# Kernel optimization log

Measured on AMD Instinct MI355X. Metric: run time of the kernel, lower is better.

The kernel has to match this reference:

```python
import jax, jax.numpy as jnp
import numpy as np

N_EMB = 768
N_HEAD = 12
B, T = 2, 2048
LN_EPS = 1e-5


def _ln(x, g, b):
    mu = jnp.mean(x, axis=-1, keepdims=True)
    var = jnp.mean((x - mu) ** 2, axis=-1, keepdims=True)
    return (x - mu) * jax.lax.rsqrt(var + LN_EPS) * g + b


def setup_inputs() -> dict:
    key = jax.random.key(0)
    ks = jax.random.split(key, 12)
    s = 0.02
    d = {
        "x": jax.random.normal(ks[0], (B, T, N_EMB), dtype=jnp.float32),
        "cond_len": 256,
        "padding_mask": jax.random.randint(ks[1], (B, T), 0, 2, dtype=jnp.int32),
        "g1": jnp.ones((N_EMB,), jnp.float32),
        "bln1": jnp.zeros((N_EMB,), jnp.float32),
        "g2": jnp.ones((N_EMB,), jnp.float32),
        "bln2": jnp.zeros((N_EMB,), jnp.float32),
        "Wq": jax.random.normal(ks[2], (N_EMB, N_EMB), jnp.float32) * s,
        "bq": jnp.zeros((N_EMB,), jnp.float32),
        "Wk": jax.random.normal(ks[3], (N_EMB, N_EMB), jnp.float32) * s,
        "bk": jnp.zeros((N_EMB,), jnp.float32),
        "Wv": jax.random.normal(ks[4], (N_EMB, N_EMB), jnp.float32) * s,
        "bv": jnp.zeros((N_EMB,), jnp.float32),
        "Wp": jax.random.normal(ks[5], (N_EMB, N_EMB), jnp.float32) * s,
        "bp": jnp.zeros((N_EMB,), jnp.float32),
        "W1": jax.random.normal(ks[6], (4 * N_EMB, N_EMB), jnp.float32) * s,
        "b1": jnp.zeros((4 * N_EMB,), jnp.float32),
        "W2": jax.random.normal(ks[7], (N_EMB, 4 * N_EMB), jnp.float32) * s,
        "b2": jnp.zeros((N_EMB,), jnp.float32),
    }
    return d


def reference(x, cond_len, padding_mask, g1, bln1, g2, bln2,
              Wq, bq, Wk, bk, Wv, bv, Wp, bp, W1, b1, W2, b2):
    Bc, Tc, C = x.shape
    H = N_HEAD
    Dh = C // H
    h = _ln(x, g1, bln1)
    q = (h @ Wq.T + bq).reshape(Bc, Tc, H, Dh)
    k = (h @ Wk.T + bk).reshape(Bc, Tc, H, Dh)
    v = (h @ Wv.T + bv).reshape(Bc, Tc, H, Dh)
    att = jnp.einsum("bqhd,bkhd->bhqk", q, k) * (1.0 / np.sqrt(Dh))
    # mask: key col allowed if col >= cond_len OR col < n_b, n_b = T - sum(pmask_b)
    n = Tc - jnp.sum(padding_mask, axis=1)  # [B]
    cols = jnp.arange(Tc)
    allowed = (cols[None, :] >= cond_len) | (cols[None, :] < n[:, None])  # [B,T]
    att = jnp.where(allowed[:, None, None, :], att, -jnp.inf)
    att = jax.nn.softmax(att, axis=-1)
    y = jnp.einsum("bhqk,bkhd->bqhd", att, v).reshape(Bc, Tc, C)
    x = x + (y @ Wp.T + bp)
    h2 = _ln(x, g2, bln2)
    m = jax.nn.gelu(h2 @ W1.T + b1, approximate=False) @ W2.T + b2
    return x + m
```

## Files before the change

### kernel.cpp

```cpp
#include <hip/hip_runtime.h>
#include <hip/hip_bf16.h>
#include <math.h>

typedef short bf16x8 __attribute__((ext_vector_type(8)));
typedef float f32x4 __attribute__((ext_vector_type(4)));
typedef unsigned short us4 __attribute__((ext_vector_type(4)));

#define MFMA(a, b, c) __builtin_amdgcn_mfma_f32_16x16x32_bf16(a, b, c, 0, 0, 0)

__device__ __forceinline__ unsigned short f2b(float f) {
  unsigned int u = __builtin_bit_cast(unsigned int, f);
  u += 0x7fffu + ((u >> 16) & 1u);
  return (unsigned short)(u >> 16);
}

__device__ __forceinline__ void gload16(const void* g, void* l) {
  __builtin_amdgcn_global_load_lds((const unsigned int*)g, (unsigned int*)l, 16, 0, 0);
}

__global__ void cvt_k(const float* __restrict__ src, unsigned short* __restrict__ dst, int n4) {
  int i = blockIdx.x * 256 + threadIdx.x;
  if (i >= n4) return;
  float4 v = ((const float4*)src)[i];
  us4 o; o.x = f2b(v.x); o.y = f2b(v.y); o.z = f2b(v.z); o.w = f2b(v.w);
  ((us4*)dst)[i] = o;
}

__global__ void cvt_qkv_k(const float* __restrict__ wq, const float* __restrict__ wk,
                          const float* __restrict__ wv, unsigned short* __restrict__ dst) {
  int i = blockIdx.x * 256 + threadIdx.x;
  if (i >= 2304 * 768 / 4) return;
  int e = i * 4;
  const float* src = e < 589824 ? wq + e : (e < 1179648 ? wk + (e - 589824) : wv + (e - 1179648));
  float4 v = *(const float4*)src;
  us4 o; o.x = f2b(v.x); o.y = f2b(v.y); o.z = f2b(v.z); o.w = f2b(v.w);
  ((us4*)dst)[i] = o;
}

__global__ void maskbias_k(const int* __restrict__ pm, const int* __restrict__ clp,
                           float* __restrict__ bias) {
  const int b = blockIdx.x, tid = threadIdx.x;
  int s = 0;
  for (int i = tid; i < 2048; i += 256) s += pm[b * 2048 + i];
  #pragma unroll
  for (int d = 1; d < 64; d <<= 1) s += __shfl_xor(s, d);
  __shared__ int red[4];
  if ((tid & 63) == 0) red[tid >> 6] = s;
  __syncthreads();
  const int n = 2048 - (red[0] + red[1] + red[2] + red[3]);
  const int cl = *clp;
  for (int t = tid; t < 2048; t += 256)
    bias[b * 2048 + t] = (t >= cl || t < n) ? 0.0f : -1e30f;
}

__global__ __launch_bounds__(256)
void ln_k(const float* __restrict__ x, const float* __restrict__ g,
          const float* __restrict__ be, unsigned short* __restrict__ out) {
  const int row = blockIdx.x * 4 + (threadIdx.x >> 6);
  const int l = threadIdx.x & 63;
  const float4* xr = (const float4*)(x + (size_t)row * 768);
  float4 v[3];
  float s = 0.f, s2 = 0.f;
  #pragma unroll
  for (int j = 0; j < 3; ++j) {
    v[j] = xr[l + j * 64];
    s += v[j].x + v[j].y + v[j].z + v[j].w;
    s2 += v[j].x * v[j].x + v[j].y * v[j].y + v[j].z * v[j].z + v[j].w * v[j].w;
  }
  #pragma unroll
  for (int d = 1; d < 64; d <<= 1) { s += __shfl_xor(s, d); s2 += __shfl_xor(s2, d); }
  const float mu = s * (1.0f / 768.0f);
  const float rstd = rsqrtf(s2 * (1.0f / 768.0f) - mu * mu + 1e-5f);
  #pragma unroll
  for (int j = 0; j < 3; ++j) {
    int c0 = (l + j * 64) * 4;
    us4 ov;
    ov.x = f2b((v[j].x - mu) * rstd * g[c0 + 0] + be[c0 + 0]);
    ov.y = f2b((v[j].y - mu) * rstd * g[c0 + 1] + be[c0 + 1]);
    ov.z = f2b((v[j].z - mu) * rstd * g[c0 + 2] + be[c0 + 2]);
    ov.w = f2b((v[j].w - mu) * rstd * g[c0 + 3] + be[c0 + 3]);
    *(us4*)(out + (size_t)row * 768 + c0) = ov;
  }
}

template<int MODE>
__global__ __launch_bounds__(256)
void gemm_k(const unsigned short* __restrict__ A, const unsigned short* __restrict__ W,
            const float* __restrict__ bias0, const float* __restrict__ bias1,
            const float* __restrict__ bias2, const float* __restrict__ resid,
            void* __restrict__ out, unsigned short* __restrict__ out2, int N, int K) {
  __shared__ __align__(16) unsigned short At[128 * 32];
  __shared__ __align__(16) unsigned short Wt[128 * 32];
  const int m0 = blockIdx.y * 128;
  const int n0 = blockIdx.x * 128;
  const int tid = threadIdx.x;
  const int w = tid >> 6, l = tid & 63;
  const int wm = w >> 1, wn = w & 1;
  const int lr = l & 15, lg = l >> 4;
  f32x4 acc[4][4] = {};

  const int nkt = K >> 5;
  for (int kt = 0; kt < nkt; ++kt) {
    const int k0 = kt << 5;
    #pragma unroll
    for (int i = 0; i < 2; ++i) {
      int slot = (i * 4 + w) * 64 + l;
      int row = slot >> 2, c8 = (slot & 3) << 3;
      gload16(A + (size_t)(m0 + row) * K + k0 + c8, (char*)At + ((i * 4 + w) * 64) * 16);
      gload16(W + (size_t)(n0 + row) * K + k0 + c8, (char*)Wt + ((i * 4 + w) * 64) * 16);
    }
    __syncthreads();
    bf16x8 af[4], bf[4];
    #pragma unroll
    for (int i = 0; i < 4; ++i) {
      af[i] = *(const bf16x8*)&At[(wm * 64 + i * 16 + lr) * 32 + lg * 8];
      bf[i] = *(const bf16x8*)&Wt[(wn * 64 + i * 16 + lr) * 32 + lg * 8];
    }
    #pragma unroll
    for (int mi = 0; mi < 4; ++mi)
      #pragma unroll
      for (int ni = 0; ni < 4; ++ni)
        acc[mi][ni] = MFMA(af[mi], bf[ni], acc[mi][ni]);
    __syncthreads();
  }

  #pragma unroll
  for (int mi = 0; mi < 4; ++mi) {
    #pragma unroll
    for (int ni = 0; ni < 4; ++ni) {
      #pragma unroll
      for (int r = 0; r < 4; ++r) {
        int row = m0 + wm * 64 + mi * 16 + lg * 4 + r;
        int col = n0 + wn * 64 + ni * 16 + lr;
        float v = acc[mi][ni][r];
        if (MODE == 0) {
          float bb = col < 768 ? bias0[col] : (col < 1536 ? bias1[col - 768] : bias2[col - 1536]);
          v += bb;
          if (col < 1536) {
            ((unsigned short*)out)[(size_t)row * 2304 + col] = f2b(v);
          } else {
            int cc = col - 1536;
            int d = cc & 63, hh = cc >> 6;
            int b = row >> 11, t = row & 2047;
            out2[(((size_t)b * 12 + hh) * 64 + d) * 2048 + t] = f2b(v);
          }
        } else if (MODE == 1) {
          v += bias0[col] + resid[(size_t)row * N + col];
          ((float*)out)[(size_t)row * N + col] = v;
        } else {
          v += bias0[col];
          v = 0.5f * v * (1.0f + erff(v * 0.70710678118f));
          ((unsigned short*)out)[(size_t)row * N + col] = f2b(v);
        }
      }
    }
  }
}

__global__ __launch_bounds__(256)
void attn_k(const unsigned short* __restrict__ qkv, const unsigned short* __restrict__ vt,
            const float* __restrict__ abias, unsigned short* __restrict__ y) {
  __shared__ __align__(16) unsigned short Kt[64 * 64];
  __shared__ __align__(16) unsigned short Vt[64 * 64];
  __shared__ __align__(16) unsigned short Pl[4][16 * 64];
  const int tile = blockIdx.x, h = blockIdx.y, b = blockIdx.z;
  const int tid = threadIdx.x, w = tid >> 6, l = tid & 63;
  const int lr = l & 15, lg = l >> 4;
  const int tq0 = tile * 64 + w * 16;

  bf16x8 qf[2];
  {
    const unsigned short* qrow = qkv + ((size_t)b * 2048 + tq0 + lr) * 2304 + h * 64;
    qf[0] = *(const bf16x8*)(qrow + lg * 8);
    qf[1] = *(const bf16x8*)(qrow + 32 + lg * 8);
  }
  f32x4 o[4] = {};
  float mrow[4] = {-1e30f, -1e30f, -1e30f, -1e30f};
  float lrow[4] = {0.f, 0.f, 0.f, 0.f};

  const unsigned short* Kg = qkv + (size_t)b * 2048 * 2304 + 768 + h * 64;
  const unsigned short* Vg = vt + ((size_t)b * 12 + h) * 64 * 2048;

  for (int kt = 0; kt < 32; ++kt) {
    const int t0 = kt * 64;
    __syncthreads();
    #pragma unroll
    for (int i = 0; i < 2; ++i) {
      int slot = (i * 4 + w) * 64 + l;
      int row = slot >> 3;
      int cc = (slot & 7) ^ (row & 7);
      gload16(Kg + (size_t)(t0 + row) * 2304 + cc * 8, (char*)Kt + ((i * 4 + w) * 64) * 16);
      gload16(Vg + (size_t)row * 2048 + t0 + cc * 8, (char*)Vt + ((i * 4 + w) * 64) * 16);
    }
    __syncthreads();

    f32x4 s[4] = {};
    #pragma unroll
    for (int kk = 0; kk < 2; ++kk)
      #pragma unroll
      for (int sub = 0; sub < 4; ++sub) {
        int trow = sub * 16 + lr;
        int boff = (trow * 128 + kk * 64 + lg * 16) ^ ((trow & 7) << 4);
        bf16x8 kf = *(const bf16x8*)((const char*)Kt + boff);
        s[sub] = MFMA(qf[kk], kf, s[sub]);
      }

    float bb[4];
    #pragma unroll
    for (int sub = 0; sub < 4; ++sub) bb[sub] = abias[b * 2048 + t0 + sub * 16 + lr];
    #pragma unroll
    for (int sub = 0; sub < 4; ++sub)
      #pragma unroll
      for (int r = 0; r < 4; ++r)
        s[sub][r] = s[sub][r] * 0.125f + bb[sub];

    float mx[4];
    #pragma unroll
    for (int r = 0; r < 4; ++r)
      mx[r] = fmaxf(fmaxf(s[0][r], s[1][r]), fmaxf(s[2][r], s[3][r]));
    #pragma unroll
    for (int d = 1; d < 16; d <<= 1)
      #pragma unroll
      for (int r = 0; r < 4; ++r)
        mx[r] = fmaxf(mx[r], __shfl_xor(mx[r], d, 16));

    float corr[4], rs[4] = {0.f, 0.f, 0.f, 0.f};
    #pragma unroll
    for (int r = 0; r < 4; ++r) {
      float mn = fmaxf(mrow[r], mx[r]);
      corr[r] = __expf(mrow[r] - mn);
      mrow[r] = mn;
    }
    #pragma unroll
    for (int sub = 0; sub < 4; ++sub)
      #pragma unroll
      for (int r = 0; r < 4; ++r) {
        float p = __expf(s[sub][r] - mrow[r]);
        s[sub][r] = p;
        rs[r] += p;
      }
    #pragma unroll
    for (int d = 1; d < 16; d <<= 1)
      #pragma unroll
      for (int r = 0; r < 4; ++r)
        rs[r] += __shfl_xor(rs[r], d, 16);
    #pragma unroll
    for (int r = 0; r < 4; ++r)
      lrow[r] = lrow[r] * corr[r] + rs[r];
    #pragma unroll
    for (int ds_ = 0; ds_ < 4; ++ds_)
      #pragma unroll
      for (int r = 0; r < 4; ++r)
        o[ds_][r] *= corr[r];

    #pragma unroll
    for (int sub = 0; sub < 4; ++sub)
      #pragma unroll
      for (int r = 0; r < 4; ++r) {
        int prow = lg * 4 + r;
        int boff = (prow * 128 + (sub * 16 + lr) * 2) ^ ((prow & 7) << 4);
        *(unsigned short*)((char*)Pl[w] + boff) = f2b(s[sub][r]);
      }

    #pragma unroll
    for (int kk = 0; kk < 2; ++kk) {
      int aoff = (lr * 128 + kk * 64 + lg * 16) ^ ((lr & 7) << 4);
      bf16x8 pa = *(const bf16x8*)((const char*)Pl[w] + aoff);
      #pragma unroll
      for (int ds_ = 0; ds_ < 4; ++ds_) {
        int vrow = ds_ * 16 + lr;
        int voff = (vrow * 128 + kk * 64 + lg * 16) ^ ((vrow & 7) << 4);
        bf16x8 vf = *(const bf16x8*)((const char*)Vt + voff);
        o[ds_] = MFMA(pa, vf, o[ds_]);
      }
    }
  }

  #pragma unroll
  for (int ds_ = 0; ds_ < 4; ++ds_)
    #pragma unroll
    for (int r = 0; r < 4; ++r) {
      int row = tq0 + lg * 4 + r;
      int col = ds_ * 16 + lr;
      y[((size_t)b * 2048 + row) * 768 + h * 64 + col] = f2b(o[ds_][r] / lrow[r]);
    }
}

extern "C" void kernel_launch(void* const* d_in, const int* in_sizes, int n_in,
                              void* d_out, int out_size, void* d_ws, size_t ws_size,
                              hipStream_t stream) {
  const float* x    = (const float*)d_in[0];
  const int* condp  = (const int*)d_in[1];
  const int* pmask  = (const int*)d_in[2];
  const float* g1   = (const float*)d_in[3];
  const float* bln1 = (const float*)d_in[4];
  const float* g2   = (const float*)d_in[5];
  const float* bln2 = (const float*)d_in[6];
  const float* Wq   = (const float*)d_in[7];
  const float* bq   = (const float*)d_in[8];
  const float* Wk   = (const float*)d_in[9];
  const float* bk   = (const float*)d_in[10];
  const float* Wv   = (const float*)d_in[11];
  const float* bv   = (const float*)d_in[12];
  const float* Wp   = (const float*)d_in[13];
  const float* bp   = (const float*)d_in[14];
  const float* W1   = (const float*)d_in[15];
  const float* b1   = (const float*)d_in[16];
  const float* W2   = (const float*)d_in[17];
  const float* b2   = (const float*)d_in[18];

  char* p = (char*)d_ws;
  auto alloc = [&](size_t bytes) { char* r = p; p += (bytes + 255) & ~(size_t)255; return r; };
  unsigned short* Wqkv = (unsigned short*)alloc((size_t)2304 * 768 * 2);
  unsigned short* Wpb  = (unsigned short*)alloc((size_t)589824 * 2);
  unsigned short* W1b  = (unsigned short*)alloc((size_t)2359296 * 2);
  unsigned short* W2b  = (unsigned short*)alloc((size_t)2359296 * 2);
  unsigned short* hb   = (unsigned short*)alloc((size_t)4096 * 768 * 2);
  unsigned short* qkv  = (unsigned short*)alloc((size_t)4096 * 2304 * 2);
  unsigned short* vtb  = (unsigned short*)alloc((size_t)24 * 64 * 2048 * 2);
  unsigned short* yb   = (unsigned short*)alloc((size_t)4096 * 768 * 2);
  float* xmid          = (float*)alloc((size_t)4096 * 768 * 4);
  unsigned short* h2b  = (unsigned short*)alloc((size_t)4096 * 768 * 2);
  unsigned short* mlph = (unsigned short*)alloc((size_t)4096 * 3072 * 2);
  float* abias         = (float*)alloc((size_t)2 * 2048 * 4);

  cvt_qkv_k<<<(2304 * 768 / 4 + 255) / 256, 256, 0, stream>>>(Wq, Wk, Wv, Wqkv);
  cvt_k<<<(589824 / 4 + 255) / 256, 256, 0, stream>>>(Wp, Wpb, 589824 / 4);
  cvt_k<<<(2359296 / 4 + 255) / 256, 256, 0, stream>>>(W1, W1b, 2359296 / 4);
  cvt_k<<<(2359296 / 4 + 255) / 256, 256, 0, stream>>>(W2, W2b, 2359296 / 4);
  maskbias_k<<<2, 256, 0, stream>>>(pmask, condp, abias);
  ln_k<<<1024, 256, 0, stream>>>(x, g1, bln1, hb);
  gemm_k<0><<<dim3(18, 32), 256, 0, stream>>>(hb, Wqkv, bq, bk, bv, nullptr, qkv, vtb, 2304, 768);
  attn_k<<<dim3(32, 12, 2), 256, 0, stream>>>(qkv, vtb, abias, yb);
  gemm_k<1><<<dim3(6, 32), 256, 0, stream>>>(yb, Wpb, bp, nullptr, nullptr, x, xmid, nullptr, 768, 768);
  ln_k<<<1024, 256, 0, stream>>>(xmid, g2, bln2, h2b);
  gemm_k<2><<<dim3(24, 32), 256, 0, stream>>>(h2b, W1b, b1, nullptr, nullptr, nullptr, mlph, nullptr, 3072, 768);
  gemm_k<1><<<dim3(6, 32), 256, 0, stream>>>(mlph, W2b, b2, nullptr, nullptr, xmid, (float*)d_out, nullptr, 768, 3072);
}
```

Measured before the change: 397.3 us.

## Split attention over keys with 32x32 MFMA and split-K output GEMMs

Attention is rewritten to use 32x32x16 MFMA with 512-thread blocks. The key dimension is split into four chunks whose partial outputs are merged by a separate combine kernel, and probabilities are packed in registers through lane shuffles instead of going through LDS. The projection and MLP-down GEMMs become split-K over four slices with fp32 partials, reduced in a fused bias+residual+LayerNorm kernel and a final combine kernel. The weight conversions are merged into fewer launches and buffers are aliased. This raises parallelism for the narrow N=768 GEMMs and for attention, at the cost of extra partial-buffer traffic and more kernel launches.

```diff
diff --git a/kernel.cpp b/kernel.cpp
--- a/kernel.cpp
+++ b/kernel.cpp
@@ -4,9 +4,11 @@
 
 typedef short bf16x8 __attribute__((ext_vector_type(8)));
 typedef float f32x4 __attribute__((ext_vector_type(4)));
+typedef float f32x16 __attribute__((ext_vector_type(16)));
 typedef unsigned short us4 __attribute__((ext_vector_type(4)));
 
-#define MFMA(a, b, c) __builtin_amdgcn_mfma_f32_16x16x32_bf16(a, b, c, 0, 0, 0)
+#define MFMA16(a, b, c) __builtin_amdgcn_mfma_f32_16x16x32_bf16(a, b, c, 0, 0, 0)
+#define MFMA32(a, b, c) __builtin_amdgcn_mfma_f32_32x32x16_bf16(a, b, c, 0, 0, 0)
 
 __device__ __forceinline__ unsigned short f2b(float f) {
   unsigned int u = __builtin_bit_cast(unsigned int, f);
@@ -14,16 +16,19 @@
   return (unsigned short)(u >> 16);
 }
 
+__device__ __forceinline__ float b2f(unsigned short u) {
+  unsigned int x = ((unsigned int)u) << 16;
+  return __builtin_bit_cast(float, x);
+}
+
+__device__ __forceinline__ unsigned int cvtpk(float lo, float hiv) {
+  unsigned int r;
+  asm("v_cvt_pk_bf16_f32 %0, %1, %2" : "=v"(r) : "v"(lo), "v"(hiv));
+  return r;
+}
+
 __device__ __forceinline__ void gload16(const void* g, void* l) {
   __builtin_amdgcn_global_load_lds((const unsigned int*)g, (unsigned int*)l, 16, 0, 0);
-}
-
-__global__ void cvt_k(const float* __restrict__ src, unsigned short* __restrict__ dst, int n4) {
-  int i = blockIdx.x * 256 + threadIdx.x;
-  if (i >= n4) return;
-  float4 v = ((const float4*)src)[i];
-  us4 o; o.x = f2b(v.x); o.y = f2b(v.y); o.z = f2b(v.z); o.w = f2b(v.w);
-  ((us4*)dst)[i] = o;
 }
 
 __global__ void cvt_qkv_k(const float* __restrict__ wq, const float* __restrict__ wk,
@@ -37,6 +42,23 @@
   ((us4*)dst)[i] = o;
 }
 
+__global__ void cvt3_k(const float* __restrict__ s0, const float* __restrict__ s1,
+                       const float* __restrict__ s2, unsigned short* __restrict__ d0,
+                       unsigned short* __restrict__ d1, unsigned short* __restrict__ d2) {
+  const int n0 = 147456, n1 = 589824, n2 = 589824;
+  int i = blockIdx.x * 256 + threadIdx.x;
+  const float* s; unsigned short* d; int j = i;
+  if (j < n0) { s = s0; d = d0; }
+  else {
+    j -= n0;
+    if (j < n1) { s = s1; d = d1; }
+    else { j -= n1; if (j >= n2) return; s = s2; d = d2; }
+  }
+  float4 v = ((const float4*)s)[j];
+  us4 o; o.x = f2b(v.x); o.y = f2b(v.y); o.z = f2b(v.z); o.w = f2b(v.w);
+  ((us4*)d)[j] = o;
+}
+
 __global__ void maskbias_k(const int* __restrict__ pm, const int* __restrict__ clp,
                            float* __restrict__ bias) {
   const int b = blockIdx.x, tid = threadIdx.x;
@@ -87,8 +109,8 @@
 __global__ __launch_bounds__(256)
 void gemm_k(const unsigned short* __restrict__ A, const unsigned short* __restrict__ W,
             const float* __restrict__ bias0, const float* __restrict__ bias1,
-            const float* __restrict__ bias2, const float* __restrict__ resid,
-            void* __restrict__ out, unsigned short* __restrict__ out2, int N, int K) {
+            const float* __restrict__ bias2, void* __restrict__ out,
+            unsigned short* __restrict__ out2, int N, int K) {
   __shared__ __align__(16) unsigned short At[128 * 32];
   __shared__ __align__(16) unsigned short Wt[128 * 32];
   const int m0 = blockIdx.y * 128;
@@ -120,7 +142,7 @@
     for (int mi = 0; mi < 4; ++mi)
       #pragma unroll
       for (int ni = 0; ni < 4; ++ni)
-        acc[mi][ni] = MFMA(af[mi], bf[ni], acc[mi][ni]);
+        acc[mi][ni] = MFMA16(af[mi], bf[ni], acc[mi][ni]);
     __syncthreads();
   }
 
@@ -144,9 +166,6 @@
             int b = row >> 11, t = row & 2047;
             out2[(((size_t)b * 12 + hh) * 64 + d) * 2048 + t] = f2b(v);
           }
-        } else if (MODE == 1) {
-          v += bias0[col] + resid[(size_t)row * N + col];
-          ((float*)out)[(size_t)row * N + col] = v;
         } else {
           v += bias0[col];
           v = 0.5f * v * (1.0f + erff(v * 0.70710678118f));
@@ -158,132 +177,272 @@
 }
 
 __global__ __launch_bounds__(256)
+void gemm_pk(const unsigned short* __restrict__ A, const unsigned short* __restrict__ W,
+             float* __restrict__ part, int N, int K, int KS) {
+  __shared__ __align__(16) unsigned short At[128 * 32];
+  __shared__ __align__(16) unsigned short Wt[128 * 32];
+  const int m0 = blockIdx.y * 128;
+  const int n0 = blockIdx.x * 128;
+  const int kb = blockIdx.z * KS;
+  const int tid = threadIdx.x;
+  const int w = tid >> 6, l = tid & 63;
+  const int wm = w >> 1, wn = w & 1;
+  const int lr = l & 15, lg = l >> 4;
+  f32x4 acc[4][4] = {};
+
+  const int nkt = KS >> 5;
+  for (int kt = 0; kt < nkt; ++kt) {
+    const int k0 = kb + (kt << 5);
+    #pragma unroll
+    for (int i = 0; i < 2; ++i) {
+      int slot = (i * 4 + w) * 64 + l;
+      int row = slot >> 2, c8 = (slot & 3) << 3;
+      gload16(A + (size_t)(m0 + row) * K + k0 + c8, (char*)At + ((i * 4 + w) * 64) * 16);
+      gload16(W + (size_t)(n0 + row) * K + k0 + c8, (char*)Wt + ((i * 4 + w) * 64) * 16);
+    }
+    __syncthreads();
+    bf16x8 af[4], bf[4];
+    #pragma unroll
+    for (int i = 0; i < 4; ++i) {
+      af[i] = *(const bf16x8*)&At[(wm * 64 + i * 16 + lr) * 32 + lg * 8];
+      bf[i] = *(const bf16x8*)&Wt[(wn * 64 + i * 16 + lr) * 32 + lg * 8];
+    }
+    #pragma unroll
+    for (int mi = 0; mi < 4; ++mi)
+      #pragma unroll
+      for (int ni = 0; ni < 4; ++ni)
+        acc[mi][ni] = MFMA16(af[mi], bf[ni], acc[mi][ni]);
+    __syncthreads();
+  }
+
+  #pragma unroll
+  for (int mi = 0; mi < 4; ++mi)
+    #pragma unroll
+    for (int ni = 0; ni < 4; ++ni)
+      #pragma unroll
+      for (int r = 0; r < 4; ++r) {
+        int row = m0 + wm * 64 + mi * 16 + lg * 4 + r;
+        int col = n0 + wn * 64 + ni * 16 + lr;
+        part[((size_t)blockIdx.z * 4096 + row) * N + col] = acc[mi][ni][r];
+      }
+}
+
+__global__ __launch_bounds__(512, 4)
 void attn_k(const unsigned short* __restrict__ qkv, const unsigned short* __restrict__ vt,
-            const float* __restrict__ abias, unsigned short* __restrict__ y) {
+            const float* __restrict__ abias, unsigned short* __restrict__ opart,
+            float* __restrict__ mpart, float* __restrict__ lpart) {
   __shared__ __align__(16) unsigned short Kt[64 * 64];
   __shared__ __align__(16) unsigned short Vt[64 * 64];
-  __shared__ __align__(16) unsigned short Pl[4][16 * 64];
-  const int tile = blockIdx.x, h = blockIdx.y, b = blockIdx.z;
+  __shared__ __align__(16) float absh[512];
+  const int d0 = blockIdx.x;
+  const int c = d0 & 7, t_ = d0 >> 3;
+  const int G = (t_ >> 3) * 8 + c;
+  const int qt = t_ & 7;
+  const int bh = G >> 2, split = G & 3;
+  const int b = bh / 12, h = bh - b * 12;
+  const int q0 = qt * 256;
+  const int tb = split * 512;
   const int tid = threadIdx.x, w = tid >> 6, l = tid & 63;
-  const int lr = l & 15, lg = l >> 4;
-  const int tq0 = tile * 64 + w * 16;
-
-  bf16x8 qf[2];
+  const int ql = l & 31, hi = l >> 5;
+  const int q = q0 + w * 32 + ql;
+
+  absh[tid] = abias[b * 2048 + tb + tid];
+
+  bf16x8 qf[4];
   {
-    const unsigned short* qrow = qkv + ((size_t)b * 2048 + tq0 + lr) * 2304 + h * 64;
-    qf[0] = *(const bf16x8*)(qrow + lg * 8);
-    qf[1] = *(const bf16x8*)(qrow + 32 + lg * 8);
-  }
-  f32x4 o[4] = {};
-  float mrow[4] = {-1e30f, -1e30f, -1e30f, -1e30f};
-  float lrow[4] = {0.f, 0.f, 0.f, 0.f};
-
-  const unsigned short* Kg = qkv + (size_t)b * 2048 * 2304 + 768 + h * 64;
-  const unsigned short* Vg = vt + ((size_t)b * 12 + h) * 64 * 2048;
-
-  for (int kt = 0; kt < 32; ++kt) {
-    const int t0 = kt * 64;
+    const unsigned short* qrow = qkv + ((size_t)b * 2048 + q) * 2304 + h * 64 + hi * 8;
+    #pragma unroll
+    for (int ds = 0; ds < 4; ++ds) qf[ds] = *(const bf16x8*)(qrow + ds * 16);
+  }
+
+  f32x16 o0 = {}, o1 = {};
+  float mrow = -1e30f, lrow = 0.f;
+
+  const int srow = tid >> 3;
+  const int scc = (tid & 7) ^ (srow & 7);
+  const unsigned short* KgL = qkv + ((size_t)b * 2048 + tb + srow) * 2304 + 768 + h * 64 + scc * 8;
+  const unsigned short* VgL = vt + ((size_t)bh * 64 + srow) * 2048 + tb + scc * 8;
+  char* KtW = (char*)Kt + w * 1024;
+  char* VtW = (char*)Vt + w * 1024;
+
+  for (int tt = 0; tt < 8; ++tt) {
+    gload16(KgL + (size_t)(tt * 64) * 2304, KtW);
+    gload16(VgL + tt * 64, VtW);
     __syncthreads();
-    #pragma unroll
-    for (int i = 0; i < 2; ++i) {
-      int slot = (i * 4 + w) * 64 + l;
-      int row = slot >> 3;
-      int cc = (slot & 7) ^ (row & 7);
-      gload16(Kg + (size_t)(t0 + row) * 2304 + cc * 8, (char*)Kt + ((i * 4 + w) * 64) * 16);
-      gload16(Vg + (size_t)row * 2048 + t0 + cc * 8, (char*)Vt + ((i * 4 + w) * 64) * 16);
-    }
+
+    f32x16 sa0 = {}, sa1 = {};
+    {
+      const int r0 = ql, r1 = 32 + ql;
+      #pragma unroll
+      for (int ds = 0; ds < 4; ++ds) {
+        bf16x8 kf0 = *(const bf16x8*)((const char*)Kt + r0 * 128 + (((ds * 2 + hi) ^ (r0 & 7)) << 4));
+        bf16x8 kf1 = *(const bf16x8*)((const char*)Kt + r1 * 128 + (((ds * 2 + hi) ^ (r1 & 7)) << 4));
+        sa0 = MFMA32(kf0, qf[ds], sa0);
+        sa1 = MFMA32(kf1, qf[ds], sa1);
+      }
+    }
+
+    float mt = -1e30f;
+    #pragma unroll
+    for (int g = 0; g < 4; ++g) {
+      float4 b0 = *(const float4*)&absh[tt * 64 + g * 8 + hi * 4];
+      float4 b1 = *(const float4*)&absh[tt * 64 + 32 + g * 8 + hi * 4];
+      float bb0[4] = {b0.x, b0.y, b0.z, b0.w};
+      float bb1[4] = {b1.x, b1.y, b1.z, b1.w};
+      #pragma unroll
+      for (int r2 = 0; r2 < 4; ++r2) {
+        float v0 = sa0[g * 4 + r2] * 0.125f + bb0[r2];
+        float v1 = sa1[g * 4 + r2] * 0.125f + bb1[r2];
+        sa0[g * 4 + r2] = v0; sa1[g * 4 + r2] = v1;
+        mt = fmaxf(mt, fmaxf(v0, v1));
+      }
+    }
+    mt = fmaxf(mt, __shfl_xor(mt, 32));
+
+    const bool grow = mt > mrow;
+    const float mnew = grow ? mt : mrow;
+    const float corr = __expf(mrow - mnew);
+    mrow = mnew;
+    if (__any((int)grow)) {
+      #pragma unroll
+      for (int g = 0; g < 4; ++g)
+        #pragma unroll
+        for (int r2 = 0; r2 < 4; ++r2) {
+          float cc2 = __shfl(corr, g * 8 + hi * 4 + r2);
+          o0[g * 4 + r2] *= cc2;
+          o1[g * 4 + r2] *= cc2;
+        }
+    }
+
+    float rs = 0.f;
+    auto half_pv = [&](const f32x16& sv, int ksb) {
+      unsigned int u[8];
+      #pragma unroll
+      for (int g = 0; g < 4; ++g) {
+        float e0 = __expf(sv[g * 4 + 0] - mnew);
+        float e1 = __expf(sv[g * 4 + 1] - mnew);
+        float e2 = __expf(sv[g * 4 + 2] - mnew);
+        float e3 = __expf(sv[g * 4 + 3] - mnew);
+        rs += (e0 + e1) + (e2 + e3);
+        u[g * 2]     = cvtpk(e0, e1);
+        u[g * 2 + 1] = cvtpk(e2, e3);
+      }
+      #pragma unroll
+      for (int kh = 0; kh < 2; ++kh) {
+        unsigned int a0 = u[kh * 4 + 0], a1 = u[kh * 4 + 1];
+        unsigned int c0 = u[kh * 4 + 2], c1 = u[kh * 4 + 3];
+        unsigned int xa0 = (unsigned int)__shfl_xor((int)a0, 32);
+        unsigned int xa1 = (unsigned int)__shfl_xor((int)a1, 32);
+        unsigned int xc0 = (unsigned int)__shfl_xor((int)c0, 32);
+        unsigned int xc1 = (unsigned int)__shfl_xor((int)c1, 32);
+        uint4 pk;
+        pk.x = hi ? xc0 : a0;
+        pk.y = hi ? xc1 : a1;
+        pk.z = hi ? c0 : xa0;
+        pk.w = hi ? c1 : xa1;
+        bf16x8 pa = __builtin_bit_cast(bf16x8, pk);
+        const int ks = ksb + kh;
+        const int vr0 = ql, vr1 = 32 + ql;
+        bf16x8 vf0 = *(const bf16x8*)((const char*)Vt + vr0 * 128 + (((ks * 2 + hi) ^ (vr0 & 7)) << 4));
+        o0 = MFMA32(pa, vf0, o0);
+        bf16x8 vf1 = *(const bf16x8*)((const char*)Vt + vr1 * 128 + (((ks * 2 + hi) ^ (vr1 & 7)) << 4));
+        o1 = MFMA32(pa, vf1, o1);
+      }
+    };
+    half_pv(sa0, 0);
+    half_pv(sa1, 2);
+
+    rs += __shfl_xor(rs, 32);
+    lrow = lrow * corr + rs;
     __syncthreads();
-
-    f32x4 s[4] = {};
-    #pragma unroll
-    for (int kk = 0; kk < 2; ++kk)
-      #pragma unroll
-      for (int sub = 0; sub < 4; ++sub) {
-        int trow = sub * 16 + lr;
-        int boff = (trow * 128 + kk * 64 + lg * 16) ^ ((trow & 7) << 4);
-        bf16x8 kf = *(const bf16x8*)((const char*)Kt + boff);
-        s[sub] = MFMA(qf[kk], kf, s[sub]);
-      }
-
-    float bb[4];
-    #pragma unroll
-    for (int sub = 0; sub < 4; ++sub) bb[sub] = abias[b * 2048 + t0 + sub * 16 + lr];
-    #pragma unroll
-    for (int sub = 0; sub < 4; ++sub)
-      #pragma unroll
-      for (int r = 0; r < 4; ++r)
-        s[sub][r] = s[sub][r] * 0.125f + bb[sub];
-
-    float mx[4];
-    #pragma unroll
-    for (int r = 0; r < 4; ++r)
-      mx[r] = fmaxf(fmaxf(s[0][r], s[1][r]), fmaxf(s[2][r], s[3][r]));
-    #pragma unroll
-    for (int d = 1; d < 16; d <<= 1)
-      #pragma unroll
-      for (int r = 0; r < 4; ++r)
-        mx[r] = fmaxf(mx[r], __shfl_xor(mx[r], d, 16));
-
-    float corr[4], rs[4] = {0.f, 0.f, 0.f, 0.f};
-    #pragma unroll
-    for (int r = 0; r < 4; ++r) {
-      float mn = fmaxf(mrow[r], mx[r]);
-      corr[r] = __expf(mrow[r] - mn);
-      mrow[r] = mn;
-    }
-    #pragma unroll
-    for (int sub = 0; sub < 4; ++sub)
-      #pragma unroll
-      for (int r = 0; r < 4; ++r) {
-        float p = __expf(s[sub][r] - mrow[r]);
-        s[sub][r] = p;
-        rs[r] += p;
-      }
-    #pragma unroll
-    for (int d = 1; d < 16; d <<= 1)
-      #pragma unroll
-      for (int r = 0; r < 4; ++r)
-        rs[r] += __shfl_xor(rs[r], d, 16);
-    #pragma unroll
-    for (int r = 0; r < 4; ++r)
-      lrow[r] = lrow[r] * corr[r] + rs[r];
-    #pragma unroll
-    for (int ds_ = 0; ds_ < 4; ++ds_)
-      #pragma unroll
-      for (int r = 0; r < 4; ++r)
-        o[ds_][r] *= corr[r];
-
-    #pragma unroll
-    for (int sub = 0; sub < 4; ++sub)
-      #pragma unroll
-      for (int r = 0; r < 4; ++r) {
-        int prow = lg * 4 + r;
-        int boff = (prow * 128 + (sub * 16 + lr) * 2) ^ ((prow & 7) << 4);
-        *(unsigned short*)((char*)Pl[w] + boff) = f2b(s[sub][r]);
-      }
-
-    #pragma unroll
-    for (int kk = 0; kk < 2; ++kk) {
-      int aoff = (lr * 128 + kk * 64 + lg * 16) ^ ((lr & 7) << 4);
-      bf16x8 pa = *(const bf16x8*)((const char*)Pl[w] + aoff);
-      #pragma unroll
-      for (int ds_ = 0; ds_ < 4; ++ds_) {
-        int vrow = ds_ * 16 + lr;
-        int voff = (vrow * 128 + kk * 64 + lg * 16) ^ ((vrow & 7) << 4);
-        bf16x8 vf = *(const bf16x8*)((const char*)Vt + voff);
-        o[ds_] = MFMA(pa, vf, o[ds_]);
-      }
-    }
-  }
-
-  #pragma unroll
-  for (int ds_ = 0; ds_ < 4; ++ds_)
-    #pragma unroll
-    for (int r = 0; r < 4; ++r) {
-      int row = tq0 + lg * 4 + r;
-      int col = ds_ * 16 + lr;
-      y[((size_t)b * 2048 + row) * 768 + h * 64 + col] = f2b(o[ds_][r] / lrow[r]);
-    }
+  }
+
+  const size_t orow0 = (size_t)split * 49152 + (size_t)bh * 2048 + q0 + w * 32;
+  if (hi == 0) { mpart[orow0 + ql] = mrow; lpart[orow0 + ql] = lrow; }
+  #pragma unroll
+  for (int g = 0; g < 4; ++g)
+    #pragma unroll
+    for (int r2 = 0; r2 < 4; ++r2) {
+      int oq = r2 + g * 8 + hi * 4;
+      opart[(orow0 + oq) * 64 + ql]      = f2b(o0[g * 4 + r2]);
+      opart[(orow0 + oq) * 64 + 32 + ql] = f2b(o1[g * 4 + r2]);
+    }
+}
+
+__global__ __launch_bounds__(256)
+void attn_comb_k(const unsigned short* __restrict__ op, const float* __restrict__ mp,
+                 const float* __restrict__ lp, unsigned short* __restrict__ y) {
+  const int row = blockIdx.x * 4 + (threadIdx.x >> 6);
+  const int l = threadIdx.x & 63;
+  float m0 = mp[row], m1 = mp[49152 + row], m2 = mp[2 * 49152 + row], m3 = mp[3 * 49152 + row];
+  float M = fmaxf(fmaxf(m0, m1), fmaxf(m2, m3));
+  float w0 = __expf(m0 - M), w1 = __expf(m1 - M), w2 = __expf(m2 - M), w3 = __expf(m3 - M);
+  float den = w0 * lp[row] + w1 * lp[49152 + row] + w2 * lp[2 * 49152 + row] + w3 * lp[3 * 49152 + row];
+  float num = w0 * b2f(op[((size_t)0 * 49152 + row) * 64 + l])
+            + w1 * b2f(op[((size_t)1 * 49152 + row) * 64 + l])
+            + w2 * b2f(op[((size_t)2 * 49152 + row) * 64 + l])
+            + w3 * b2f(op[((size_t)3 * 49152 + row) * 64 + l]);
+  const int bh = row >> 11, qq = row & 2047;
+  const int bb = bh / 12, hh = bh - bb * 12;
+  y[((size_t)(bb * 2048 + qq)) * 768 + hh * 64 + l] = f2b(num / den);
+}
+
+__global__ __launch_bounds__(256)
+void proj_ln_k(const float* __restrict__ part, const float* __restrict__ bp,
+               const float* __restrict__ xres, const float* __restrict__ g2,
+               const float* __restrict__ bln2, float* __restrict__ xmid,
+               unsigned short* __restrict__ h2) {
+  const int row = blockIdx.x * 4 + (threadIdx.x >> 6);
+  const int l = threadIdx.x & 63;
+  float4 v[3];
+  float s = 0.f, s2 = 0.f;
+  #pragma unroll
+  for (int j = 0; j < 3; ++j) {
+    const int cc = l + j * 64;
+    float4 a = ((const float4*)(xres + (size_t)row * 768))[cc];
+    float4 bb = ((const float4*)bp)[cc];
+    a.x += bb.x; a.y += bb.y; a.z += bb.z; a.w += bb.w;
+    #pragma unroll
+    for (int sp = 0; sp < 4; ++sp) {
+      float4 pp = ((const float4*)(part + ((size_t)sp * 4096 + row) * 768))[cc];
+      a.x += pp.x; a.y += pp.y; a.z += pp.z; a.w += pp.w;
+    }
+    v[j] = a;
+    s += a.x + a.y + a.z + a.w;
+    s2 += a.x * a.x + a.y * a.y + a.z * a.z + a.w * a.w;
+  }
+  #pragma unroll
+  for (int d = 1; d < 64; d <<= 1) { s += __shfl_xor(s, d); s2 += __shfl_xor(s2, d); }
+  const float mu = s * (1.0f / 768.0f);
+  const float rstd = rsqrtf(s2 * (1.0f / 768.0f) - mu * mu + 1e-5f);
+  #pragma unroll
+  for (int j = 0; j < 3; ++j) {
+    const int cc = l + j * 64;
+    ((float4*)(xmid + (size_t)row * 768))[cc] = v[j];
+    const int c0 = cc * 4;
+    us4 ov;
+    ov.x = f2b((v[j].x - mu) * rstd * g2[c0 + 0] + bln2[c0 + 0]);
+    ov.y = f2b((v[j].y - mu) * rstd * g2[c0 + 1] + bln2[c0 + 1]);
+    ov.z = f2b((v[j].z - mu) * rstd * g2[c0 + 2] + bln2[c0 + 2]);
+    ov.w = f2b((v[j].w - mu) * rstd * g2[c0 + 3] + bln2[c0 + 3]);
+    *(us4*)(h2 + (size_t)row * 768 + c0) = ov;
+  }
+}
+
+__global__ void mlp2_comb_k(const float* __restrict__ part, const float* __restrict__ b2,
+                            const float* __restrict__ xmid, float* __restrict__ out) {
+  const int i = blockIdx.x * 256 + threadIdx.x;
+  if (i >= 786432) return;
+  const int c4 = i % 192;
+  float4 a = ((const float4*)xmid)[i];
+  float4 bb = ((const float4*)b2)[c4];
+  a.x += bb.x; a.y += bb.y; a.z += bb.z; a.w += bb.w;
+  #pragma unroll
+  for (int sp = 0; sp < 4; ++sp) {
+    float4 pp = ((const float4*)part)[(size_t)sp * 786432 + i];
+    a.x += pp.x; a.y += pp.y; a.z += pp.z; a.w += pp.w;
+  }
+  ((float4*)out)[i] = a;
 }
 
 extern "C" void kernel_launch(void* const* d_in, const int* in_sizes, int n_in,
@@ -318,22 +477,26 @@
   unsigned short* hb   = (unsigned short*)alloc((size_t)4096 * 768 * 2);
   unsigned short* qkv  = (unsigned short*)alloc((size_t)4096 * 2304 * 2);
   unsigned short* vtb  = (unsigned short*)alloc((size_t)24 * 64 * 2048 * 2);
-  unsigned short* yb   = (unsigned short*)alloc((size_t)4096 * 768 * 2);
   float* xmid          = (float*)alloc((size_t)4096 * 768 * 4);
   unsigned short* h2b  = (unsigned short*)alloc((size_t)4096 * 768 * 2);
-  unsigned short* mlph = (unsigned short*)alloc((size_t)4096 * 3072 * 2);
   float* abias         = (float*)alloc((size_t)2 * 2048 * 4);
-
-  cvt_qkv_k<<<(2304 * 768 / 4 + 255) / 256, 256, 0, stream>>>(Wq, Wk, Wv, Wqkv);
-  cvt_k<<<(589824 / 4 + 255) / 256, 256, 0, stream>>>(Wp, Wpb, 589824 / 4);
-  cvt_k<<<(2359296 / 4 + 255) / 256, 256, 0, stream>>>(W1, W1b, 2359296 / 4);
-  cvt_k<<<(2359296 / 4 + 255) / 256, 256, 0, stream>>>(W2, W2b, 2359296 / 4);
+  float* partial       = (float*)alloc((size_t)4 * 4096 * 768 * 4);
+  unsigned short* yb   = hb;
+  unsigned short* mlph = qkv;
+  unsigned short* opart = (unsigned short*)partial;
+  float* mpart = (float*)((char*)partial + (size_t)4 * 49152 * 64 * 2);
+  float* lpart = mpart + 4 * 49152;
+
+  cvt_qkv_k<<<1728, 256, 0, stream>>>(Wq, Wk, Wv, Wqkv);
+  cvt3_k<<<5184, 256, 0, stream>>>(Wp, W1, W2, Wpb, W1b, W2b);
   maskbias_k<<<2, 256, 0, stream>>>(pmask, condp, abias);
   ln_k<<<1024, 256, 0, stream>>>(x, g1, bln1, hb);
-  gemm_k<0><<<dim3(18, 32), 256, 0, stream>>>(hb, Wqkv, bq, bk, bv, nullptr, qkv, vtb, 2304, 768);
-  attn_k<<<dim3(32, 12, 2), 256, 0, stream>>>(qkv, vtb, abias, yb);
-  gemm_k<1><<<dim3(6, 32), 256, 0, stream>>>(yb, Wpb, bp, nullptr, nullptr, x, xmid, nullptr, 768, 768);
-  ln_k<<<1024, 256, 0, stream>>>(xmid, g2, bln2, h2b);
-  gemm_k<2><<<dim3(24, 32), 256, 0, stream>>>(h2b, W1b, b1, nullptr, nullptr, nullptr, mlph, nullptr, 3072, 768);
-  gemm_k<1><<<dim3(6, 32), 256, 0, stream>>>(mlph, W2b, b2, nullptr, nullptr, xmid, (float*)d_out, nullptr, 768, 3072);
-}
+  gemm_k<0><<<dim3(18, 32), 256, 0, stream>>>(hb, Wqkv, bq, bk, bv, qkv, vtb, 2304, 768);
+  attn_k<<<768, 512, 0, stream>>>(qkv, vtb, abias, opart, mpart, lpart);
+  attn_comb_k<<<12288, 256, 0, stream>>>(opart, mpart, lpart, yb);
+  gemm_pk<<<dim3(6, 32, 4), 256, 0, stream>>>(yb, Wpb, partial, 768, 768, 192);
+  proj_ln_k<<<1024, 256, 0, stream>>>(partial, bp, x, g2, bln2, xmid, h2b);
+  gemm_k<2><<<dim3(24, 32), 256, 0, stream>>>(h2b, W1b, b1, nullptr, nullptr, mlph, nullptr, 3072, 768);
+  gemm_pk<<<dim3(6, 32, 4), 256, 0, stream>>>(mlph, W2b, partial, 768, 3072, 768);
+  mlp2_comb_k<<<3072, 256, 0, stream>>>(partial, b2, xmid, (float*)d_out);
+}
```

Measured after the change: 348.9 us. 1.14x faster.
